# Performance work log

Measured on AMD Instinct MI355X. Metric: run time of the kernel, lower is better.

The kernel has to match this reference:

```python
import jax, jax.numpy as jnp
import numpy as np

B, S, D_IN, D, H = 2, 2048, 1024, 1024, 16
HD = D // H

def setup_inputs() -> dict:
    key = jax.random.key(0)
    k1, k2, k3 = jax.random.split(key, 3)
    # xavier_uniform-style scale for weights
    lim_qkv = float(np.sqrt(6.0 / (D_IN + 3 * D)))
    lim_o = float(np.sqrt(6.0 / (D + D)))
    return {
        "x": jax.random.normal(k1, (B, S, D_IN), dtype=jnp.float32),
        "w_qkv": jax.random.uniform(k2, (3 * D, D_IN), dtype=jnp.float32, minval=-lim_qkv, maxval=lim_qkv),
        "b_qkv": jnp.zeros((3 * D,), dtype=jnp.float32),
        "w_o": jax.random.uniform(k3, (D, D), dtype=jnp.float32, minval=-lim_o, maxval=lim_o),
        "b_o": jnp.zeros((D,), dtype=jnp.float32),
    }

def reference(x, w_qkv, b_qkv, w_o, b_o):
    b, s, _ = x.shape
    # QKV projection: [B,S,3D]
    qkv = jnp.einsum("bsd,ed->bse", x, w_qkv) + b_qkv
    # [B,S,H,3*HD] -> [B,H,S,3*HD]
    qkv = qkv.reshape(b, s, H, 3 * HD).transpose(0, 2, 1, 3)
    q, k, v = jnp.split(qkv, 3, axis=-1)  # each [B,H,S,HD]
    scale = 1.0 / jnp.sqrt(jnp.asarray(HD, dtype=q.dtype))
    logits = jnp.einsum("bhqd,bhkd->bhqk", q, k) * scale  # [B,H,S,S]
    attn = jax.nn.softmax(logits, axis=-1)
    vals = jnp.einsum("bhqk,bhkd->bhqd", attn, v)  # [B,H,S,HD]
    vals = vals.transpose(0, 2, 1, 3).reshape(b, s, D)
    return jnp.einsum("bsd,ed->bse", vals, w_o) + b_o
```

## Files before the change

kernel.cpp:

```cpp
#include <hip/hip_runtime.h>
#include <hip/hip_bf16.h>
#include <math.h>

#define BATCH 2
#define SLEN  2048
#define DIN   1024
#define DMODEL 1024
#define NHEAD 16
#define HD    64
#define E3    3072

typedef unsigned short us;
typedef _Float16 f16;
typedef __attribute__((ext_vector_type(8))) _Float16 f16x8;
typedef __attribute__((ext_vector_type(8))) unsigned short us8;
typedef __attribute__((ext_vector_type(4))) unsigned short us4;
typedef __attribute__((ext_vector_type(4))) float f32x4;
typedef __attribute__((ext_vector_type(16))) float f32x16;
typedef __attribute__((ext_vector_type(4))) unsigned int u32x4;

#define QSCALE 0.18033688011112042f

__device__ __forceinline__ us f16bits(float x) {
    const f16 h = (f16)x;
    return __builtin_bit_cast(us, h);
}

__device__ __forceinline__ unsigned int pkrtz(float a, float b) {
    return __builtin_bit_cast(unsigned int, __builtin_amdgcn_cvt_pkrtz(a, b));
}

__device__ __forceinline__ void plswap(unsigned int& a, unsigned int& b) {
    asm volatile("v_permlane32_swap_b32 %0, %1" : "+v"(a), "+v"(b));
}

__device__ __forceinline__ void barrier_raw() {
    asm volatile("s_barrier" ::: "memory");
}

#define GLL16(g, l)                                                                     \
    __builtin_amdgcn_global_load_lds((const __attribute__((address_space(1))) unsigned int*)(g), \
                                     (__attribute__((address_space(3))) unsigned int*)(l), 16, 0, 0)

__global__ __launch_bounds__(256) void cvt3_f16(
    const float* __restrict__ x, us* __restrict__ ox, int nx,
    const float* __restrict__ wq, us* __restrict__ owq, int nq,
    const float* __restrict__ wo, us* __restrict__ owo)
{
    int i = (blockIdx.x * 256 + threadIdx.x) * 8;
    const float* s;
    us* o;
    if (i < nx)           { s = x;  o = ox; }
    else if (i < nx + nq) { s = wq; o = owq; i -= nx; }
    else                  { s = wo; o = owo; i -= nx + nq; }
    const float4 f0 = *(const float4*)&s[i];
    const float4 f1 = *(const float4*)&s[i + 4];
    const float v[8] = {f0.x, f0.y, f0.z, f0.w, f1.x, f1.y, f1.z, f1.w};
    us8 h;
#pragma unroll
    for (int j = 0; j < 8; ++j) h[j] = f16bits(v[j]);
    *(us8*)&o[i] = h;
}

#define G2BK 64

template <bool QKV_OUT>
__global__ __launch_bounds__(512, 1) void gemm256_f16(
    const us* __restrict__ Am, const us* __restrict__ Bm,
    const float* __restrict__ bias, void* __restrict__ Cout,
    int M, int N, int K)
{
    __shared__ __align__(16) us ldsA[2 * 256 * 64];
    __shared__ __align__(16) us ldsB[2 * 256 * 64];

    const int t    = threadIdx.x;
    const int lane = t & 63;
    const int w    = t >> 6;
    const int ml   = lane & 15;
    const int quad = lane >> 4;
    const int msk  = ml & 7;
    const int wm   = w >> 2;
    const int wn   = w & 3;
    const int GNT  = K / G2BK;

    const int nbx = N >> 8;
    const int nwg = (M >> 8) * nbx;
    int wg = blockIdx.y * nbx + blockIdx.x;
    wg = (wg & 7) * (nwg >> 3) + (wg >> 3);
    const int m0 = (wg / nbx) * 256;
    const int n0 = (wg % nbx) * 256;

    const int r8  = lane >> 3;
    const int xsw = ((lane & 7) ^ r8) * 8;
    const us* pA = Am + (size_t)(m0 + w * 32 + r8) * K + xsw;
    const us* pB = Bm + (size_t)(n0 + w * 32 + r8) * K + xsw;

#define STG_A(d, kk) do { _Pragma("unroll") for (int g = 0; g < 4; ++g) \
    GLL16(pA + (size_t)(8 * g) * K + (kk), &ldsA[(d) * 16384 + w * 2048 + g * 512]); } while (0)
#define STG_B(d, kk) do { _Pragma("unroll") for (int g = 0; g < 4; ++g) \
    GLL16(pB + (size_t)(8 * g) * K + (kk), &ldsB[(d) * 16384 + w * 2048 + g * 512]); } while (0)

#define LDA(d, mi, ks) __builtin_bit_cast(f16x8, *(const us8*)&ldsA[(d) * 16384 + (wm * 128 + (mi) * 16 + ml) * 64 + (((quad ^ msk) ^ ((ks) << 2)) * 8)])
#define LDB(d, nj, ks) __builtin_bit_cast(f16x8, *(const us8*)&ldsB[(d) * 16384 + (wn * 64 + (nj) * 16 + ml) * 64 + (((quad ^ msk) ^ ((ks) << 2)) * 8)])

    f32x4 acc[8][4];
#pragma unroll
    for (int i = 0; i < 8; ++i)
#pragma unroll
        for (int j = 0; j < 4; ++j) {
            acc[i][j][0] = 0.f; acc[i][j][1] = 0.f; acc[i][j][2] = 0.f; acc[i][j][3] = 0.f;
        }

    STG_A(0, 0); STG_B(0, 0);
    STG_B(1, G2BK);
    asm volatile("s_waitcnt vmcnt(4)" ::: "memory");
    barrier_raw();

    for (int tt = 0; tt < GNT; ++tt) {
        const int d = tt & 1, e = d ^ 1;

        if (tt + 1 < GNT) STG_A(e, (tt + 1) * G2BK);
        f16x8 bf[2][4];
#pragma unroll
        for (int ks = 0; ks < 2; ++ks)
#pragma unroll
            for (int nj = 0; nj < 4; ++nj)
                bf[ks][nj] = LDB(d, nj, ks);
        f16x8 af[4][2];
#pragma unroll
        for (int mi = 0; mi < 4; ++mi) {
            af[mi][0] = LDA(d, mi, 0);
            af[mi][1] = LDA(d, mi, 1);
        }
        __builtin_amdgcn_s_setprio(1);
#pragma unroll
        for (int ks = 0; ks < 2; ++ks)
#pragma unroll
            for (int nj = 0; nj < 4; ++nj)
#pragma unroll
                for (int mi = 0; mi < 4; ++mi)
                    acc[mi][nj] = __builtin_amdgcn_mfma_f32_16x16x32_f16(af[mi][ks], bf[ks][nj], acc[mi][nj], 0, 0, 0);
        __builtin_amdgcn_s_setprio(0);
        barrier_raw();

        if (tt + 2 < GNT) STG_B(d, (tt + 2) * G2BK);
#pragma unroll
        for (int mi = 0; mi < 4; ++mi) {
            af[mi][0] = LDA(d, mi + 4, 0);
            af[mi][1] = LDA(d, mi + 4, 1);
        }
        __builtin_amdgcn_s_setprio(1);
#pragma unroll
        for (int ks = 0; ks < 2; ++ks)
#pragma unroll
            for (int nj = 0; nj < 4; ++nj)
#pragma unroll
                for (int mi = 0; mi < 4; ++mi)
                    acc[mi + 4][nj] = __builtin_amdgcn_mfma_f32_16x16x32_f16(af[mi][ks], bf[ks][nj], acc[mi + 4][nj], 0, 0, 0);
        __builtin_amdgcn_s_setprio(0);

        if (tt + 2 < GNT)      asm volatile("s_waitcnt vmcnt(4)" ::: "memory");
        else if (tt + 1 < GNT) asm volatile("s_waitcnt vmcnt(0)" ::: "memory");
        barrier_raw();
    }

    float bj[4], cs[4];
#pragma unroll
    for (int nj = 0; nj < 4; ++nj) {
        const int col = n0 + wn * 64 + nj * 16 + ml;
        bj[nj] = bias[col];
        cs[nj] = (QKV_OUT && (col % 192) < 64) ? QSCALE : 1.0f;
    }
#pragma unroll
    for (int mi = 0; mi < 8; ++mi) {
#pragma unroll
        for (int r = 0; r < 4; ++r) {
            const size_t rowoff = (size_t)(m0 + wm * 128 + mi * 16 + quad * 4 + r) * N;
#pragma unroll
            for (int nj = 0; nj < 4; ++nj) {
                const int col = n0 + wn * 64 + nj * 16 + ml;
                const float v = (acc[mi][nj][r] + bj[nj]) * cs[nj];
                if (QKV_OUT) ((us*)Cout)[rowoff + col] = f16bits(v);
                else         ((float*)Cout)[rowoff + col] = v;
            }
        }
    }
#undef STG_A
#undef STG_B
#undef LDA
#undef LDB
}

#define GBK 64
#define GNT (DIN / GBK)

template <int BN, bool QKV_OUT>
__global__ __launch_bounds__(256) void gemm_db(
    const us* __restrict__ Am, const us* __restrict__ Bm,
    const float* __restrict__ bias, void* __restrict__ Cout,
    int M, int N, int K)
{
    constexpr int NJ  = BN / 32;
    constexpr int BGL = BN / 32;
    __shared__ __align__(16) us ldsA[2 * 128 * 64];
    __shared__ __align__(16) us ldsB[2 * BN * 64];

    const int t    = threadIdx.x;
    const int lane = t & 63;
    const int w    = t >> 6;
    const int ml   = lane & 15;
    const int quad = lane >> 4;
    const int msk  = ml & 7;
    const int wm   = w >> 1;
    const int wn   = w & 1;

    const int nbx = N / BN;
    const int nwg = (M >> 7) * nbx;
    int wg = blockIdx.y * nbx + blockIdx.x;
    wg = (wg & 7) * (nwg >> 3) + (wg >> 3);
    const int m0 = (wg / nbx) * 128;
    const int n0 = (wg % nbx) * BN;

    const int r8  = lane >> 3;
    const int xsw = ((lane & 7) ^ r8) * 8;
    const us* pA = Am + (size_t)(m0 + w * 32 + r8) * K + xsw;
    const int brow = (BN == 128) ? w * 32 : w * 16;
    const us* pB = Bm + (size_t)(n0 + brow + r8) * K + xsw;

#define STG_A(d, kk) do { _Pragma("unroll") for (int g = 0; g < 4; ++g) \
    GLL16(pA + (size_t)(8 * g) * K + (kk), &ldsA[(d) * 8192 + w * 2048 + g * 512]); } while (0)
#define STG_B(d, kk) do { _Pragma("unroll") for (int g = 0; g < BGL; ++g) \
    GLL16(pB + (size_t)(8 * g) * K + (kk), &ldsB[(d) * (BN * 64) + brow * 64 + g * 512]); } while (0)

#define LDA(d, mi, ks) __builtin_bit_cast(f16x8, *(const us8*)&ldsA[(d) * 8192 + (wm * 64 + (mi) * 16 + ml) * 64 + (((quad ^ msk) ^ ((ks) << 2)) * 8)])
#define LDB(d, nj, ks) __builtin_bit_cast(f16x8, *(const us8*)&ldsB[(d) * (BN * 64) + (wn * (BN / 2) + (nj) * 16 + ml) * 64 + (((quad ^ msk) ^ ((ks) << 2)) * 8)])

#define WAIT_BGL() do { if constexpr (BN == 128) asm volatile("s_waitcnt vmcnt(4)" ::: "memory"); \
                        else                     asm volatile("s_waitcnt vmcnt(2)" ::: "memory"); } while (0)

    f32x4 acc[4][NJ];
#pragma unroll
    for (int i = 0; i < 4; ++i)
#pragma unroll
        for (int j = 0; j < NJ; ++j) {
            acc[i][j][0] = 0.f; acc[i][j][1] = 0.f; acc[i][j][2] = 0.f; acc[i][j][3] = 0.f;
        }

    STG_A(0, 0); STG_B(0, 0);
    STG_B(1, GBK);
    WAIT_BGL();
    barrier_raw();

    for (int tt = 0; tt < GNT; ++tt) {
        const int d = tt & 1, e = d ^ 1;

        if (tt + 1 < GNT) STG_A(e, (tt + 1) * GBK);
        f16x8 bf[2][NJ];
#pragma unroll
        for (int ks = 0; ks < 2; ++ks)
#pragma unroll
            for (int nj = 0; nj < NJ; ++nj)
                bf[ks][nj] = LDB(d, nj, ks);
        f16x8 a0[2][2];
#pragma unroll
        for (int mi = 0; mi < 2; ++mi) {
            a0[mi][0] = LDA(d, mi, 0);
            a0[mi][1] = LDA(d, mi, 1);
        }
        __builtin_amdgcn_s_setprio(1);
#pragma unroll
        for (int ks = 0; ks < 2; ++ks)
#pragma unroll
            for (int nj = 0; nj < NJ; ++nj)
#pragma unroll
                for (int mi = 0; mi < 2; ++mi)
                    acc[mi][nj] = __builtin_amdgcn_mfma_f32_16x16x32_f16(a0[mi][ks], bf[ks][nj], acc[mi][nj], 0, 0, 0);
        __builtin_amdgcn_s_setprio(0);
        barrier_raw();

        if (tt + 2 < GNT) STG_B(d, (tt + 2) * GBK);
        f16x8 a1[2][2];
#pragma unroll
        for (int mi = 0; mi < 2; ++mi) {
            a1[mi][0] = LDA(d, mi + 2, 0);
            a1[mi][1] = LDA(d, mi + 2, 1);
        }
        __builtin_amdgcn_s_setprio(1);
#pragma unroll
        for (int ks = 0; ks < 2; ++ks)
#pragma unroll
            for (int nj = 0; nj < NJ; ++nj)
#pragma unroll
                for (int mi = 0; mi < 2; ++mi)
                    acc[mi + 2][nj] = __builtin_amdgcn_mfma_f32_16x16x32_f16(a1[mi][ks], bf[ks][nj], acc[mi + 2][nj], 0, 0, 0);
        __builtin_amdgcn_s_setprio(0);

        if (tt + 2 < GNT)      WAIT_BGL();
        else if (tt + 1 < GNT) asm volatile("s_waitcnt vmcnt(0)" ::: "memory");
        barrier_raw();
    }

    float bj[NJ], cs[NJ];
#pragma unroll
    for (int nj = 0; nj < NJ; ++nj) {
        const int col = n0 + wn * (BN / 2) + nj * 16 + ml;
        bj[nj] = bias[col];
        cs[nj] = (QKV_OUT && (col % 192) < 64) ? QSCALE : 1.0f;
    }
#pragma unroll
    for (int mi = 0; mi < 4; ++mi) {
#pragma unroll
        for (int r = 0; r < 4; ++r) {
            const size_t rowoff = (size_t)(m0 + wm * 64 + mi * 16 + quad * 4 + r) * N;
#pragma unroll
            for (int nj = 0; nj < NJ; ++nj) {
                const int col = n0 + wn * (BN / 2) + nj * 16 + ml;
                const float v = (acc[mi][nj][r] + bj[nj]) * cs[nj];
                if (QKV_OUT) ((us*)Cout)[rowoff + col] = f16bits(v);
                else         ((float*)Cout)[rowoff + col] = v;
            }
        }
    }
#undef STG_A
#undef STG_B
#undef LDA
#undef LDB
#undef WAIT_BGL
}

#define ABQ 128
#define ACH 64
#define NCH (SLEN / ACH)
#define NCH2 (NCH / 2)
#define LQA 72
#define OSTR 68

__global__ __launch_bounds__(512, 2) void attn_mfma(
    const us* __restrict__ qkvh, us* __restrict__ vals)
{
    __shared__ __align__(16) us smem[36864];

    const int t    = threadIdx.x;
    const int lane = t & 63;
    const int w    = t >> 6;
    const int sp   = w >> 2;
    const int wq4  = w & 3;
    const int t2   = t & 255;
    const int m32  = lane & 31;
    const int half = lane >> 5;

    const int wg  = blockIdx.x;
    const int s9  = wg >> 3;
    const int bh  = ((s9 >> 4) << 3) | (wg & 7);
    const int b   = bh >> 4;
    const int h   = bh & 15;
    const int q0  = (s9 & 15) * ABQ;

    const size_t base = (size_t)b * SLEN * E3;
    const int qoff = h * 192;

    const int krA = t2 >> 2;
    const int ksA = (t2 & 3) * 16;
    const int k2  = t2 & 31;
    const int d0v = (t2 >> 5) * 8;

    us* const Kb0 = smem + sp * 4608;
    us* const Kb1 = smem + 9216 + sp * 4608;
    us* const Vb0 = smem + 18432 + sp * 4608;
    us* const Vb1 = smem + 27648 + sp * 4608;
    const int cg0 = sp * NCH2;

    us8 kk0, kk1, vv0, vv1;
#define LOADKV(cgi) do { \
    const us* gK = &qkvh[base + (size_t)((cgi) * ACH + krA) * E3 + qoff + 64 + ksA]; \
    kk0 = *(const us8*)gK; kk1 = *(const us8*)(gK + 8); \
    const us* gV = &qkvh[base + (size_t)((cgi) * ACH + 2 * k2) * E3 + qoff + 128 + d0v]; \
    vv0 = *(const us8*)gV; vv1 = *(const us8*)(gV + E3); } while (0)

    LOADKV(cg0);
    {
        const int row = t >> 2;
        const int c0q = (t & 3) * 16;
        const us* g = &qkvh[base + (size_t)(q0 + row) * E3 + qoff + c0q];
        *(us8*)&smem[row * LQA + c0q]     = *(const us8*)g;
        *(us8*)&smem[row * LQA + c0q + 8] = *(const us8*)(g + 8);
    }
    __syncthreads();

    f16x8 aq[4];
#pragma unroll
    for (int s = 0; s < 4; ++s)
        aq[s] = __builtin_bit_cast(f16x8, *(const us8*)&smem[(wq4 * 32 + m32) * LQA + half * 8 + 16 * s]);
    __syncthreads();

    *(us8*)&Kb0[krA * LQA + ksA]     = kk0;
    *(us8*)&Kb0[krA * LQA + ksA + 8] = kk1;
#pragma unroll
    for (int j = 0; j < 8; ++j) {
        const unsigned int pv = (unsigned int)vv0[j] | ((unsigned int)vv1[j] << 16);
        *(unsigned int*)&Vb0[(d0v + j) * LQA + 2 * k2] = pv;
    }
    LOADKV(cg0 + 1);
    __syncthreads();

    f32x16 O[2];
#pragma unroll
    for (int dt = 0; dt < 2; ++dt)
#pragma unroll
        for (int r = 0; r < 16; ++r) O[dt][r] = 0.f;
    float lp[2] = {0.f, 0.f};

    for (int c = 0; c < NCH2; ++c) {
        us* const Krd = (c & 1) ? Kb1 : Kb0;
        us* const Vrd = (c & 1) ? Vb1 : Vb0;
        us* const Kwr = (c & 1) ? Kb0 : Kb1;
        us* const Vwr = (c & 1) ? Vb0 : Vb1;

        if (c + 1 < NCH2) {
            *(us8*)&Kwr[krA * LQA + ksA]     = kk0;
            *(us8*)&Kwr[krA * LQA + ksA + 8] = kk1;
#pragma unroll
            for (int j = 0; j < 8; ++j) {
                const unsigned int pv = (unsigned int)vv0[j] | ((unsigned int)vv1[j] << 16);
                *(unsigned int*)&Vwr[(d0v + j) * LQA + 2 * k2] = pv;
            }
        }
        if (c + 2 < NCH2) LOADKV(cg0 + c + 2);

        f16x8 pf[4];
#pragma unroll
        for (int kt = 0; kt < 2; ++kt) {
            f32x16 z;
#pragma unroll
            for (int r = 0; r < 16; ++r) z[r] = 0.f;
            __builtin_amdgcn_s_setprio(1);
#pragma unroll
            for (int s = 0; s < 4; ++s) {
                const f16x8 ak = __builtin_bit_cast(f16x8, *(const us8*)&Krd[(kt * 32 + m32) * LQA + half * 8 + 16 * s]);
                z = __builtin_amdgcn_mfma_f32_32x32x16_f16(ak, aq[s], z, 0, 0, 0);
            }
            __builtin_amdgcn_s_setprio(0);
            {
                float p[8];
#pragma unroll
                for (int r = 0; r < 8; ++r) {
                    p[r] = __builtin_amdgcn_exp2f(z[r]);
                    lp[r & 1] += p[r];
                }
                unsigned int a0 = pkrtz(p[0], p[1]), a1 = pkrtz(p[2], p[3]);
                unsigned int b0 = pkrtz(p[4], p[5]), b1 = pkrtz(p[6], p[7]);
                plswap(a0, b0); plswap(a1, b1);
                pf[2 * kt] = __builtin_bit_cast(f16x8, (u32x4){a0, a1, b0, b1});
            }
            {
                float p[8];
#pragma unroll
                for (int r = 0; r < 8; ++r) {
                    p[r] = __builtin_amdgcn_exp2f(z[8 + r]);
                    lp[r & 1] += p[r];
                }
                unsigned int e0 = pkrtz(p[0], p[1]), e1 = pkrtz(p[2], p[3]);
                unsigned int f0 = pkrtz(p[4], p[5]), f1 = pkrtz(p[6], p[7]);
                plswap(e0, f0); plswap(e1, f1);
                pf[2 * kt + 1] = __builtin_bit_cast(f16x8, (u32x4){e0, e1, f0, f1});
            }
        }

        __builtin_amdgcn_s_setprio(1);
#pragma unroll
        for (int dt = 0; dt < 2; ++dt) {
#pragma unroll
            for (int s = 0; s < 4; ++s) {
                const f16x8 av = __builtin_bit_cast(f16x8, *(const us8*)&Vrd[(dt * 32 + m32) * LQA + half * 8 + 16 * s]);
                O[dt] = __builtin_amdgcn_mfma_f32_32x32x16_f16(av, pf[s], O[dt], 0, 0, 0);
            }
        }
        __builtin_amdgcn_s_setprio(0);

        __syncthreads();
    }

    const float lpart = lp[0] + lp[1];
    const float l = lpart + __shfl_xor(lpart, 32);
    const int ql = wq4 * 32 + m32;

    __syncthreads();
    float* const Osc = (float*)smem;
    float* const lsc = Osc + ABQ * OSTR;

    if (sp == 1) {
#pragma unroll
        for (int dt = 0; dt < 2; ++dt) {
#pragma unroll
            for (int g = 0; g < 4; ++g) {
                const f32x4 o4 = {O[dt][g * 4], O[dt][g * 4 + 1], O[dt][g * 4 + 2], O[dt][g * 4 + 3]};
                *(f32x4*)&Osc[ql * OSTR + dt * 32 + 8 * g + 4 * half] = o4;
            }
        }
        if (half == 0) lsc[ql] = l;
    }
    __syncthreads();
    if (sp == 0) {
        const float rl = 1.0f / (l + lsc[ql]);
        const int sq = q0 + ql;
        const size_t rowbase = (size_t)(b * SLEN + sq) * DMODEL + h * HD;
#pragma unroll
        for (int dt = 0; dt < 2; ++dt) {
#pragma unroll
            for (int g = 0; g < 4; ++g) {
                const f32x4 part = *(const f32x4*)&Osc[ql * OSTR + dt * 32 + 8 * g + 4 * half];
                us4 o4;
#pragma unroll
                for (int r2 = 0; r2 < 4; ++r2)
                    o4[r2] = f16bits((O[dt][g * 4 + r2] + part[r2]) * rl);
                *(us4*)&vals[rowbase + dt * 32 + 8 * g + 4 * half] = o4;
            }
        }
    }
#undef LOADKV
}

extern "C" void kernel_launch(void* const* d_in, const int* in_sizes, int n_in,
                              void* d_out, int out_size, void* d_ws, size_t ws_size,
                              hipStream_t stream) {
    const float* x     = (const float*)d_in[0];
    const float* w_qkv = (const float*)d_in[1];
    const float* b_qkv = (const float*)d_in[2];
    const float* w_o   = (const float*)d_in[3];
    const float* b_o   = (const float*)d_in[4];
    float* out = (float*)d_out;

    const int M   = BATCH * SLEN;
    const int XN  = M * DIN;
    const int WQN = E3 * DIN;
    const int WON = DMODEL * DMODEL;
    const size_t QKVN = (size_t)BATCH * SLEN * E3;

    us* qkvh = (us*)d_ws;
    us* xh   = qkvh + QKVN;
    us* wq   = xh + XN;
    us* wo   = wq + WQN;

    cvt3_f16<<<dim3((XN + WQN + WON) / 2048), 256, 0, stream>>>(
        x, xh, XN, w_qkv, wq, WQN, w_o, wo);

    gemm256_f16<true><<<dim3(E3 / 256, M / 256), 512, 0, stream>>>(
        xh, wq, b_qkv, qkvh, M, E3, DIN);

    us* vals = xh;
    attn_mfma<<<dim3((SLEN / ABQ) * BATCH * NHEAD), 512, 0, stream>>>(qkvh, vals);

    gemm_db<128, false><<<dim3(DMODEL / 128, M / 128), 256, 0, stream>>>(
        vals, wo, b_o, out, M, DMODEL, DMODEL);
}
```

Baseline: 187.4 us.

## Split attention KV range across two sequential kernel launches via global partials

Replaces the single 512-thread attention kernel, which split keys between two wave groups and merged them in shared memory, with two 256-thread launches. Each launch handles half of the key chunks. The first writes unnormalized O and row sums to a global workspace, and the second adds them and normalizes. Smaller blocks with half the shared memory may allow more resident blocks per CU. The cost is an extra kernel launch, global round-trips for the fp32 partials, and no concurrency between the two key halves.

```diff
diff --git a/kernel.cpp b/kernel.cpp
--- a/kernel.cpp
+++ b/kernel.cpp
@@ -330,22 +330,19 @@
 
 #define ABQ 128
 #define ACH 64
-#define NCH (SLEN / ACH)
-#define NCH2 (NCH / 2)
+#define CHN 16
 #define LQA 72
-#define OSTR 68
-
-__global__ __launch_bounds__(512, 2) void attn_mfma(
-    const us* __restrict__ qkvh, us* __restrict__ vals)
+
+template <bool FIRST>
+__global__ __launch_bounds__(256, 4) void attn_half(
+    const us* __restrict__ qkvh, us* __restrict__ vals,
+    float* __restrict__ Opart, float* __restrict__ lpart, int cbase)
 {
-    __shared__ __align__(16) us smem[36864];
+    __shared__ __align__(16) us smem[18432];
 
     const int t    = threadIdx.x;
     const int lane = t & 63;
     const int w    = t >> 6;
-    const int sp   = w >> 2;
-    const int wq4  = w & 3;
-    const int t2   = t & 255;
     const int m32  = lane & 31;
     const int half = lane >> 5;
 
@@ -359,16 +356,15 @@
     const size_t base = (size_t)b * SLEN * E3;
     const int qoff = h * 192;
 
-    const int krA = t2 >> 2;
-    const int ksA = (t2 & 3) * 16;
-    const int k2  = t2 & 31;
-    const int d0v = (t2 >> 5) * 8;
-
-    us* const Kb0 = smem + sp * 4608;
-    us* const Kb1 = smem + 9216 + sp * 4608;
-    us* const Vb0 = smem + 18432 + sp * 4608;
-    us* const Vb1 = smem + 27648 + sp * 4608;
-    const int cg0 = sp * NCH2;
+    const int krA = t >> 2;
+    const int ksA = (t & 3) * 16;
+    const int k2  = t & 31;
+    const int d0v = (t >> 5) * 8;
+
+    us* const Kb0 = smem;
+    us* const Kb1 = smem + 4608;
+    us* const Vb0 = smem + 9216;
+    us* const Vb1 = smem + 13824;
 
     us8 kk0, kk1, vv0, vv1;
 #define LOADKV(cgi) do { \
@@ -377,20 +373,22 @@
     const us* gV = &qkvh[base + (size_t)((cgi) * ACH + 2 * k2) * E3 + qoff + 128 + d0v]; \
     vv0 = *(const us8*)gV; vv1 = *(const us8*)(gV + E3); } while (0)
 
-    LOADKV(cg0);
+    LOADKV(cbase);
     {
-        const int row = t >> 2;
-        const int c0q = (t & 3) * 16;
+        const int row = t >> 1;
+        const int c0q = (t & 1) * 32;
         const us* g = &qkvh[base + (size_t)(q0 + row) * E3 + qoff + c0q];
-        *(us8*)&smem[row * LQA + c0q]     = *(const us8*)g;
-        *(us8*)&smem[row * LQA + c0q + 8] = *(const us8*)(g + 8);
+        *(us8*)&smem[row * LQA + c0q]      = *(const us8*)g;
+        *(us8*)&smem[row * LQA + c0q + 8]  = *(const us8*)(g + 8);
+        *(us8*)&smem[row * LQA + c0q + 16] = *(const us8*)(g + 16);
+        *(us8*)&smem[row * LQA + c0q + 24] = *(const us8*)(g + 24);
     }
     __syncthreads();
 
     f16x8 aq[4];
 #pragma unroll
     for (int s = 0; s < 4; ++s)
-        aq[s] = __builtin_bit_cast(f16x8, *(const us8*)&smem[(wq4 * 32 + m32) * LQA + half * 8 + 16 * s]);
+        aq[s] = __builtin_bit_cast(f16x8, *(const us8*)&smem[(w * 32 + m32) * LQA + half * 8 + 16 * s]);
     __syncthreads();
 
     *(us8*)&Kb0[krA * LQA + ksA]     = kk0;
@@ -400,7 +398,7 @@
         const unsigned int pv = (unsigned int)vv0[j] | ((unsigned int)vv1[j] << 16);
         *(unsigned int*)&Vb0[(d0v + j) * LQA + 2 * k2] = pv;
     }
-    LOADKV(cg0 + 1);
+    LOADKV(cbase + 1);
     __syncthreads();
 
     f32x16 O[2];
@@ -410,13 +408,13 @@
         for (int r = 0; r < 16; ++r) O[dt][r] = 0.f;
     float lp[2] = {0.f, 0.f};
 
-    for (int c = 0; c < NCH2; ++c) {
+    for (int c = 0; c < CHN; ++c) {
         us* const Krd = (c & 1) ? Kb1 : Kb0;
         us* const Vrd = (c & 1) ? Vb1 : Vb0;
         us* const Kwr = (c & 1) ? Kb0 : Kb1;
         us* const Vwr = (c & 1) ? Vb0 : Vb1;
 
-        if (c + 1 < NCH2) {
+        if (c + 1 < CHN) {
             *(us8*)&Kwr[krA * LQA + ksA]     = kk0;
             *(us8*)&Kwr[krA * LQA + ksA + 8] = kk1;
 #pragma unroll
@@ -425,7 +423,7 @@
                 *(unsigned int*)&Vwr[(d0v + j) * LQA + 2 * k2] = pv;
             }
         }
-        if (c + 2 < NCH2) LOADKV(cg0 + c + 2);
+        if (c + 2 < CHN) LOADKV(cbase + c + 2);
 
         f16x8 pf[4];
 #pragma unroll
@@ -480,35 +478,30 @@
         __syncthreads();
     }
 
-    const float lpart = lp[0] + lp[1];
-    const float l = lpart + __shfl_xor(lpart, 32);
-    const int ql = wq4 * 32 + m32;
-
-    __syncthreads();
-    float* const Osc = (float*)smem;
-    float* const lsc = Osc + ABQ * OSTR;
-
-    if (sp == 1) {
+    const float lsum = lp[0] + lp[1];
+    const float l2 = lsum + __shfl_xor(lsum, 32);
+    const int sq = q0 + w * 32 + m32;
+    const size_t prow = ((size_t)bh * SLEN + sq) * HD;
+
+    if (FIRST) {
 #pragma unroll
         for (int dt = 0; dt < 2; ++dt) {
 #pragma unroll
             for (int g = 0; g < 4; ++g) {
                 const f32x4 o4 = {O[dt][g * 4], O[dt][g * 4 + 1], O[dt][g * 4 + 2], O[dt][g * 4 + 3]};
-                *(f32x4*)&Osc[ql * OSTR + dt * 32 + 8 * g + 4 * half] = o4;
-            }
-        }
-        if (half == 0) lsc[ql] = l;
-    }
-    __syncthreads();
-    if (sp == 0) {
-        const float rl = 1.0f / (l + lsc[ql]);
-        const int sq = q0 + ql;
+                *(f32x4*)&Opart[prow + dt * 32 + 8 * g + 4 * half] = o4;
+            }
+        }
+        if (half == 0) lpart[(size_t)bh * SLEN + sq] = l2;
+    } else {
+        const float lo = lpart[(size_t)bh * SLEN + sq];
+        const float rl = 1.0f / (l2 + lo);
         const size_t rowbase = (size_t)(b * SLEN + sq) * DMODEL + h * HD;
 #pragma unroll
         for (int dt = 0; dt < 2; ++dt) {
 #pragma unroll
             for (int g = 0; g < 4; ++g) {
-                const f32x4 part = *(const f32x4*)&Osc[ql * OSTR + dt * 32 + 8 * g + 4 * half];
+                const f32x4 part = *(const f32x4*)&Opart[prow + dt * 32 + 8 * g + 4 * half];
                 us4 o4;
 #pragma unroll
                 for (int r2 = 0; r2 < 4; ++r2)
@@ -540,6 +533,8 @@
     us* xh   = qkvh + QKVN;
     us* wq   = xh + XN;
     us* wo   = wq + WQN;
+    float* Opart = (float*)(wo + WON);
+    float* lpart = Opart + (size_t)BATCH * NHEAD * SLEN * HD;
 
     cvt3_f16<<<dim3((XN + WQN + WON) / 2048), 256, 0, stream>>>(
         x, xh, XN, w_qkv, wq, WQN, w_o, wo);
@@ -548,7 +543,10 @@
         xh, wq, b_qkv, qkvh, M, E3, DIN);
 
     us* vals = xh;
-    attn_mfma<<<dim3((SLEN / ABQ) * BATCH * NHEAD), 512, 0, stream>>>(qkvh, vals);
+    attn_half<true><<<dim3((SLEN / ABQ) * BATCH * NHEAD), 256, 0, stream>>>(
+        qkvh, vals, Opart, lpart, 0);
+    attn_half<false><<<dim3((SLEN / ABQ) * BATCH * NHEAD), 256, 0, stream>>>(
+        qkvh, vals, Opart, lpart, CHN);
 
     gemm_db<128, false><<<dim3(DMODEL / 128, M / 128), 256, 0, stream>>>(
         vals, wo, b_o, out, M, DMODEL, DMODEL);
```

Measured after the change: 193.8 us. +3.4%, slower.
